# Optimization experiments

Hardware: AMD Instinct MI355X
Metric: run time of the kernel (lower is better)

The kernel has to match this reference:

```python
import jax, jax.numpy as jnp
import numpy as np

K = 20          # neighbors
T = 3           # time steps
GW = 10.0       # surrogate-gradient width
EPS = 1e-5      # batchnorm eps


def _knn_idx(f, k):
    # f: (B, N, C). torch code maximizes -||xi-xj||^2 via topk.
    x2 = jnp.sum(f * f, axis=-1)                          # (B, N)
    inner = jnp.einsum('bnc,bmc->bnm', f, f)              # (B, N, N)
    neg_d = 2.0 * inner - x2[:, :, None] - x2[:, None, :]
    return jax.lax.top_k(neg_d, k)[1]                     # (B, N, k)


def _graph_feature(f, k):
    # f: (B, N, C) -> (B, N, k, 2C) = cat(neighbor - center, neighbor)
    idx = _knn_idx(f, k)
    nb = jax.vmap(lambda ft, ix: ft[ix])(f, idx)          # (B, N, k, C)
    return jnp.concatenate([nb - f[:, :, None, :], nb], axis=-1)


def _bn(x, g, b, axes):
    # training-mode batchnorm (batch statistics), channel-last
    m = jnp.mean(x, axis=axes, keepdims=True)
    v = jnp.var(x, axis=axes, keepdims=True)
    return (x - m) * jax.lax.rsqrt(v + EPS) * g + b


def _lrelu(x):
    return jnp.where(x >= 0, x, 0.2 * x)


def _spike(x):
    # surrogate value + straight-through hard spike (training-mode detach trick)
    xc = jnp.clip(x, -10.0, 10.0)
    soft = 0.5 * jnp.exp(-0.5 * xc * xc) / np.sqrt(2.0 * np.pi) + 0.5 * jax.nn.sigmoid(GW * xc)
    hard = (x > 0).astype(x.dtype)
    return soft + jax.lax.stop_gradient(hard - soft)


def _lif(x, mem, thr, ref, md, ta, rd, tb):
    md = jnp.clip(md, 0.1, 0.99)
    ta = jnp.clip(ta, 0.001, 0.1)
    rd = jnp.clip(rd, 0.1, 0.95)
    x = x * (ref <= 0).astype(x.dtype)
    mem = mem * md * (1.0 - ref) + x
    s = _spike(mem - thr)
    mem = mem * (1.0 - s)
    ref = ref * rd + s
    thr = tb + (thr + ta * s - tb) * 0.95
    return s, mem, thr, ref


def _forward(x, W0, g0, b0, W1, g1, b1, W2, g2, b2, W3, g3, b3, Wm, gm, bm,
             l0md, l0ta, l0rd, l0tb, l1md, l1ta, l1rd, l1tb,
             l2md, l2ta, l2rd, l2tb, l3md, l3ta, l3rd, l3tb,
             lfmd, lfta, lfrd, lftb, tw):
    f0 = jnp.transpose(x, (0, 2, 1))                      # (B, N, 3)
    convs = [(W0, g0, b0), (W1, g1, b1), (W2, g2, b2), (W3, g3, b3)]
    lifs = [(l0md, l0ta, l0rd, l0tb), (l1md, l1ta, l1rd, l1tb),
            (l2md, l2ta, l2rd, l2tb), (l3md, l3ta, l3rd, l3tb)]
    states = [None] * 4
    pooled = []
    for t in range(T):
        cur = f0
        feats = []
        for i in range(4):
            gf = _graph_feature(cur, K)                   # (B, N, k, 2C)
            h = jnp.einsum('bnkc,oc->bnko', gf, convs[i][0])  # 1x1 conv
            h = _lrelu(_bn(h, convs[i][1], convs[i][2], (0, 1, 2)))
            h = jnp.max(h, axis=2)                        # max over k -> (B, N, O)
            md, ta, rd, tb = lifs[i]
            if states[i] is None:
                mem = jnp.zeros_like(h)
                thr = jnp.broadcast_to(tb, h.shape).astype(h.dtype)
                ref = jnp.zeros_like(h)
            else:
                # state manager detaches persisted states between calls
                mem, thr, ref = (jax.lax.stop_gradient(s) for s in states[i])
            s, mem, thr, ref = _lif(h, mem, thr, ref, md, ta, rd, tb)
            states[i] = (mem, thr, ref)
            feats.append(s)
            cur = s
        cat = jnp.concatenate(feats, axis=-1)             # (B, N, 960)
        agg = _lrelu(_bn(jnp.einsum('bnc,oc->bno', cat, Wm), gm, bm, (0, 1)))
        pooled.append(jnp.max(agg, axis=1))               # global max pool -> (B, 512)
    tf = jnp.stack(pooled, axis=0)                        # (T, B, 512)
    out = jnp.einsum('t,tbf->bf', jax.nn.softmax(tw), tf)
    mem = jnp.zeros_like(out)
    thr = jnp.broadcast_to(lftb, out.shape).astype(out.dtype)
    ref = jnp.zeros_like(out)
    s, _, _, _ = _lif(out, mem, thr, ref, lfmd, lfta, lfrd, lftb)
    return s


def setup_inputs() -> dict:
    key = jax.random.key(0)
    ks = iter(jax.random.split(key, 64))
    B, N = 2, 1024
    d = {}
    d['x'] = jax.random.normal(next(ks), (B, 3, N), jnp.float32)
    dims = [(64, 6), (128, 128), (256, 256), (512, 512)]  # (out, in) for 1x1 convs
    for i, (o, c) in enumerate(dims):
        d[f'W{i}'] = jax.random.normal(next(ks), (o, c), jnp.float32) / np.sqrt(c)
        d[f'g{i}'] = 1.0 + 0.1 * jax.random.normal(next(ks), (o,), jnp.float32)
        d[f'b{i}'] = 0.1 * jax.random.normal(next(ks), (o,), jnp.float32)
    d['Wm'] = jax.random.normal(next(ks), (512, 960), jnp.float32) / np.sqrt(960.0)
    d['gm'] = 1.0 + 0.1 * jax.random.normal(next(ks), (512,), jnp.float32)
    d['bm'] = 0.1 * jax.random.normal(next(ks), (512,), jnp.float32)
    for name, c in [('l0', 64), ('l1', 128), ('l2', 256), ('l3', 512), ('lf', 512)]:
        d[name + 'md'] = jnp.full((c,), 0.9, jnp.float32) + 0.02 * jax.random.normal(next(ks), (c,), jnp.float32)
        d[name + 'ta'] = jnp.full((c,), 0.01, jnp.float32) + 0.002 * jax.random.normal(next(ks), (c,), jnp.float32)
        d[name + 'rd'] = jnp.full((c,), 0.5, jnp.float32) + 0.02 * jax.random.normal(next(ks), (c,), jnp.float32)
        d[name + 'tb'] = jnp.ones((c,), jnp.float32) + 0.05 * jax.random.normal(next(ks), (c,), jnp.float32)
    d['tw'] = 1.0 + 0.1 * jax.random.normal(next(ks), (T,), jnp.float32)
    return d


def reference(x, W0, g0, b0, W1, g1, b1, W2, g2, b2, W3, g3, b3, Wm, gm, bm,
              l0md, l0ta, l0rd, l0tb, l1md, l1ta, l1rd, l1tb,
              l2md, l2ta, l2rd, l2tb, l3md, l3ta, l3rd, l3tb,
              lfmd, lfta, lfrd, lftb, tw):
    return _forward(x, W0, g0, b0, W1, g1, b1, W2, g2, b2, W3, g3, b3, Wm, gm, bm,
                    l0md, l0ta, l0rd, l0tb, l1md, l1ta, l1rd, l1tb,
                    l2md, l2ta, l2rd, l2tb, l3md, l3ta, l3rd, l3tb,
                    lfmd, lfta, lfrd, lftb, tw)
```

## Files before the change

kernel.cpp:

```cpp
#include <hip/hip_runtime.h>
#include <math.h>

#define NPTS 1024
#define BB 2
#define KNN 20
#define ROWS 2048
#define CATC 960
#define TT 3
#define IDXS 32
typedef unsigned long long ull;
typedef __attribute__((ext_vector_type(8))) short bf16x8;
typedef __attribute__((ext_vector_type(4))) float f32x4;

__device__ __forceinline__ float lrelu_f(float x){ return x >= 0.f ? x : 0.2f*x; }
__device__ __forceinline__ unsigned short f2bf(float f){
  unsigned u = __float_as_uint(f);
  return (unsigned short)((u + 0x7FFFu + ((u >> 16) & 1u)) >> 16);
}
__device__ __forceinline__ float bf2f(unsigned short h){ return __uint_as_float(((unsigned)h) << 16); }

__device__ __forceinline__ void stg_u32(unsigned* p, unsigned v){ __hip_atomic_store(p, v, __ATOMIC_RELAXED, __HIP_MEMORY_SCOPE_AGENT); }
__device__ __forceinline__ void stg_f64(double* p, double v){ __hip_atomic_store(p, v, __ATOMIC_RELAXED, __HIP_MEMORY_SCOPE_AGENT); }
__device__ __forceinline__ unsigned ldg_u32(const unsigned* p){ return __hip_atomic_load(p, __ATOMIC_RELAXED, __HIP_MEMORY_SCOPE_AGENT); }
__device__ __forceinline__ double ldg_f64(const double* p){ return __hip_atomic_load(p, __ATOMIC_RELAXED, __HIP_MEMORY_SCOPE_AGENT); }

__device__ __forceinline__ void mfma_dev(const short* __restrict__ A, int lda,
    const short* __restrict__ B3, size_t sStride, int ldb,
    float* __restrict__ C, int ldc, int K, int bm, int bn, int tid)
{
  const int wave = tid >> 6, lane = tid & 63;
  const int wm = (wave >> 1) << 5, wn = (wave & 1) << 5;
  const int rr = lane & 15, kq = (lane >> 4) << 3;
  f32x4 acc[2][2] = {};
  const short* Ap = A + (size_t)(bm + wm + rr)*lda + kq;
  const short* Bp = B3 + (size_t)(bn + wn + rr)*ldb + kq;
  for (int k0 = 0; k0 < K; k0 += 32) {
    bf16x8 a0 = *(const bf16x8*)(Ap + k0);
    bf16x8 a1 = *(const bf16x8*)(Ap + (size_t)16*lda + k0);
#pragma unroll
    for (int s = 0; s < 3; ++s) {
      bf16x8 b0 = *(const bf16x8*)(Bp + (size_t)s*sStride + k0);
      bf16x8 b1 = *(const bf16x8*)(Bp + (size_t)s*sStride + (size_t)16*ldb + k0);
      acc[0][0] = __builtin_amdgcn_mfma_f32_16x16x32_bf16(a0, b0, acc[0][0], 0, 0, 0);
      acc[0][1] = __builtin_amdgcn_mfma_f32_16x16x32_bf16(a0, b1, acc[0][1], 0, 0, 0);
      acc[1][0] = __builtin_amdgcn_mfma_f32_16x16x32_bf16(a1, b0, acc[1][0], 0, 0, 0);
      acc[1][1] = __builtin_amdgcn_mfma_f32_16x16x32_bf16(a1, b1, acc[1][1], 0, 0, 0);
    }
  }
  const int drb = (lane >> 4) << 2;
#pragma unroll
  for (int i = 0; i < 2; ++i)
#pragma unroll
    for (int j = 0; j < 2; ++j)
#pragma unroll
      for (int t = 0; t < 4; ++t)
        C[(size_t)(bm + wm + i*16 + drb + t)*ldc + bn + wn + j*16 + rr] = acc[i][j][t];
}

__device__ __forceinline__ void agg_tile64(const short* __restrict__ scat, const short* __restrict__ WmH,
    double* __restrict__ Sa1, double* __restrict__ Sa2, unsigned* __restrict__ mxe,
    int tm, int tn, int tid)
{
  const int wave = tid >> 6, lane = tid & 63;
  const int wm = (wave >> 1) << 5;
  const int wn = (wave & 1) << 5;
  const int rr = lane & 15, kq = (lane >> 4) << 3;
  const int bm = tm*64, bn = tn*64;
  f32x4 acc[2][2] = {};
  const short* Ap = scat + (size_t)(bm + wm + rr)*CATC + kq;
  const short* Bp = WmH + (size_t)(bn + wn + rr)*960 + kq;
  for (int k0 = 0; k0 < 960; k0 += 32){
    bf16x8 a0 = *(const bf16x8*)(Ap + k0);
    bf16x8 a1 = *(const bf16x8*)(Ap + (size_t)16*CATC + k0);
#pragma unroll
    for (int s = 0; s < 3; ++s){
      bf16x8 b0 = *(const bf16x8*)(Bp + (size_t)s*491520 + k0);
      bf16x8 b1 = *(const bf16x8*)(Bp + (size_t)s*491520 + (size_t)16*960 + k0);
      acc[0][0] = __builtin_amdgcn_mfma_f32_16x16x32_bf16(a0, b0, acc[0][0], 0, 0, 0);
      acc[0][1] = __builtin_amdgcn_mfma_f32_16x16x32_bf16(a0, b1, acc[0][1], 0, 0, 0);
      acc[1][0] = __builtin_amdgcn_mfma_f32_16x16x32_bf16(a1, b0, acc[1][0], 0, 0, 0);
      acc[1][1] = __builtin_amdgcn_mfma_f32_16x16x32_bf16(a1, b1, acc[1][1], 0, 0, 0);
    }
  }
#pragma unroll
  for (int j = 0; j < 2; ++j){
    double ds = 0.0, dq = 0.0; float mx = -INFINITY;
#pragma unroll
    for (int i = 0; i < 2; ++i)
#pragma unroll
      for (int t = 0; t < 4; ++t){
        float v = acc[i][j][t];
        ds += (double)v; dq += (double)v*(double)v; mx = fmaxf(mx, v);
      }
#pragma unroll
    for (int off = 16; off < 64; off <<= 1){
      ds += __shfl_xor(ds, off);
      dq += __shfl_xor(dq, off);
      float o = __shfl_xor(mx, off); mx = fmaxf(mx, o);
    }
    if (lane < 16){
      int col = bn + wn + j*16 + lane;
      atomicAdd(&Sa1[col], ds);
      atomicAdd(&Sa2[col], dq);
      unsigned u = __float_as_uint(mx);
      u = (u & 0x80000000u) ? ~u : (u | 0x80000000u);
      atomicMax(&mxe[(bm >> 10)*512 + col], u);
    }
  }
}

template<int W>
__device__ __forceinline__ void knn_wave(const ull* __restrict__ pk, int* __restrict__ idx,
                                         int row, int lane)
{
  const int n = row & (NPTS-1), b = row >> 10;
  const ull* pb = pk + (size_t)b*NPTS*W;
  ull cw[W]; int pn = 0;
#pragma unroll
  for (int w=0; w<W; ++w){ cw[w] = pb[(size_t)n*W + w]; pn += __popcll(cw[w]); }
  unsigned keys[16];
#pragma unroll 4
  for (int i=0;i<16;++i){
    int m = lane + (i<<6);
    int inner=0, pm=0;
#pragma unroll
    for (int w=0;w<W;++w){
      ull rm = pb[(size_t)m*W + w];
      inner += __popcll(rm & cw[w]);
      pm    += __popcll(rm);
    }
    int d = 2*inner - pn - pm;
    keys[i] = ((unsigned)(d+1024)<<11) | (unsigned)(NPTS-1-m);
  }
  unsigned lmax = keys[0];
#pragma unroll
  for (int i=1;i<16;++i) lmax = keys[i]>lmax ? keys[i] : lmax;
  unsigned mywin = 0;
  for (int s=0;s<KNN;++s){
    unsigned v = lmax;
#pragma unroll
    for (int off=1; off<64; off<<=1){ unsigned o = __shfl_xor(v, off, 64); if (o>v) v=o; }
    if (lane == s) mywin = (unsigned)(NPTS-1) - (v & 0x7FFu);
    if (lmax == v){
#pragma unroll
      for (int i=0;i<16;++i) if (keys[i]==v) keys[i]=0u;
      lmax = keys[0];
#pragma unroll
      for (int i=1;i<16;++i) lmax = keys[i]>lmax ? keys[i] : lmax;
    }
  }
  if (lane < KNN) idx[(size_t)row*IDXS + lane] = (int)mywin;
}

__device__ __forceinline__ void knn0_wave(const float* __restrict__ x, int* __restrict__ idx,
                                          int row, int lane)
{
  const int n = row & (NPTS-1), b = row >> 10;
  const float* xb = x + (size_t)b*3*NPTS;
  float fn0 = xb[n], fn1 = xb[NPTS+n], fn2 = xb[2*NPTS+n];
  float x2n = __fadd_rn(__fadd_rn(__fmul_rn(fn0,fn0), __fmul_rn(fn1,fn1)), __fmul_rn(fn2,fn2));
  ull keys[16];
#pragma unroll 4
  for (int i=0;i<16;++i){
    int m = lane + (i<<6);
    float a0 = xb[m], a1 = xb[NPTS+m], a2 = xb[2*NPTS+m];
    float x2m = __fadd_rn(__fadd_rn(__fmul_rn(a0,a0), __fmul_rn(a1,a1)), __fmul_rn(a2,a2));
    float inner = __fadd_rn(__fadd_rn(__fmul_rn(fn0,a0), __fmul_rn(fn1,a1)), __fmul_rn(fn2,a2));
    float v = __fsub_rn(__fsub_rn(__fmul_rn(2.f,inner), x2n), x2m);
    unsigned u = __float_as_uint(v);
    u = (u & 0x80000000u) ? ~u : (u | 0x80000000u);
    keys[i] = ((ull)u << 32) | (unsigned)(NPTS-1-m);
  }
  ull lmax = keys[0];
#pragma unroll
  for (int i=1;i<16;++i) lmax = keys[i]>lmax ? keys[i] : lmax;
  unsigned mywin = 0;
  for (int s=0;s<KNN;++s){
    ull v = lmax;
#pragma unroll
    for (int off=1; off<64; off<<=1){ ull o = __shfl_xor(v, off, 64); if (o>v) v=o; }
    if (lane == s) mywin = (unsigned)(NPTS-1) - (unsigned)(v & 0xFFFFFFFFull);
    if (lmax == v){
#pragma unroll
      for (int i=0;i<16;++i) if (keys[i]==v) keys[i]=0ull;
      lmax = keys[0];
#pragma unroll
      for (int i=1;i<16;++i) lmax = keys[i]>lmax ? keys[i] : lmax;
    }
  }
  if (lane < KNN) idx[(size_t)row*IDXS + lane] = (int)mywin;
}

__device__ __forceinline__ void conv0_dev(const float* __restrict__ x, const float* __restrict__ W0,
    float* __restrict__ AB0, int tile, int tid, float* sm)
{
  float (*As)[64] = (float(*)[64])sm;
  float (*Bs)[64] = (float(*)[64])(sm + 3*64);
  int bm = (tile >> 1) * 64, bn = (tile & 1) * 64;
  int b = bm >> 10, n0 = bm & (NPTS-1);
  if (tid < 192){ int k = tid >> 6, r = tid & 63; As[k][r] = x[(size_t)b*3072 + k*NPTS + n0 + r]; }
  if (tid >= 64){
    int k = (tid - 64) >> 6, c = (tid - 64) & 63; int row = bn + c;
    Bs[k][c] = (row < 64) ? __fadd_rn(W0[(size_t)row*6+k], W0[(size_t)row*6+3+k])
                          : W0[(size_t)(row-64)*6+k];
  }
  __syncthreads();
  const int tx = tid & 15, ty = tid >> 4;
  float acc[4][4] = {};
#pragma unroll
  for (int kk = 0; kk < 3; ++kk){
    float ar[4], br[4];
#pragma unroll
    for (int i=0;i<4;++i) ar[i] = As[kk][ty*4+i];
#pragma unroll
    for (int j=0;j<4;++j) br[j] = Bs[kk][tx*4+j];
#pragma unroll
    for (int i=0;i<4;++i)
#pragma unroll
      for (int j=0;j<4;++j) acc[i][j] = fmaf(ar[i], br[j], acc[i][j]);
  }
#pragma unroll
  for (int i=0;i<4;++i)
#pragma unroll
    for (int j=0;j<4;++j)
      AB0[(size_t)(bm+ty*4+i)*128 + bn+tx*4+j] = acc[i][j];
  __syncthreads();
}

__device__ __forceinline__ void wsplit_store(float w, short* dst, size_t NK, size_t e){
  unsigned short h1 = f2bf(w); float f1 = bf2f(h1);
  float r1 = w - f1;
  unsigned short h2 = f2bf(r1); float f2v = bf2f(h2);
  unsigned short h3 = f2bf(r1 - f2v);
  dst[e] = (short)h1; dst[NK + e] = (short)h2; dst[2*NK + e] = (short)h3;
}
__device__ __forceinline__ void wcatsplit(const float* __restrict__ W, short* __restrict__ dst,
                                          int O, int C, size_t e){
  int rr = (int)(e / C), cc = (int)(e - (size_t)rr*C);
  float w = (rr < O) ? __fadd_rn(W[(size_t)rr*2*C + cc], W[(size_t)rr*2*C + C + cc])
                     : W[(size_t)(rr-O)*2*C + cc];
  wsplit_store(w, dst, (size_t)2*O*C, e);
}

__device__ __forceinline__ float lif_step(float h, int o, size_t i, int init,
    double s1v, double s2v,
    const float* gv, const float* bv,
    const float* pmd, const float* pta, const float* prd, const float* ptb,
    float* sM, float* sT, float* sR)
{
  double cnt = (double)ROWS * (double)KNN;
  double mu = s1v / cnt;
  double vv = s2v / cnt - mu*mu;
  float mean = (float)mu;
  float inv  = 1.f / sqrtf((float)vv + 1e-5f);
  h = ((h - mean) * inv) * gv[o] + bv[o];
  h = lrelu_f(h);
  float md = fminf(fmaxf(pmd[o], 0.1f), 0.99f);
  float ta = fminf(fmaxf(pta[o], 0.001f), 0.1f);
  float rd = fminf(fmaxf(prd[o], 0.1f), 0.95f);
  float tb = ptb[o];
  float M, T, R;
  if (init) { M = 0.f; T = tb; R = 0.f; }
  else      { M = sM[i]; T = sT[i]; R = sR[i]; }
  float xv = (R <= 0.f) ? h : 0.f;
  M = M * md * (1.f - R) + xv;
  float sp = (M - T > 0.f) ? 1.f : 0.f;
  M = M * (1.f - sp);
  R = R * rd + sp;
  T = tb + (T + ta*sp - tb) * 0.95f;
  sM[i] = M; sT[i] = T; sR[i] = R;
  return sp;
}
__device__ __forceinline__ void emit_spike(float sp, short* scat, size_t row, int off, int o,
                                           ull* pk, size_t i, int tid)
{
  scat[row*CATC + off + o] = (sp != 0.f) ? (short)0x3F80 : (short)0;
  ull ball = __ballot(sp != 0.f);
  if ((tid & 63) == 0) pk[i >> 6] = ball;
}

__global__ __launch_bounds__(256) void k_setup(
    const float* W1, const float* W2, const float* W3, const float* Wm,
    short* wcH1, short* wcH2, short* wcH3, short* WmH,
    double* S12all, double* aggD, unsigned* aggM, unsigned* cnt)
{
  int vb = blockIdx.x, tid = threadIdx.x;
  if (vb < 10){ for (int j=tid; j<1024; j+=256) stg_f64(S12all + (size_t)vb*1024 + j, 0.0); }
  else if (vb < 13){ int t = vb-10;
    for (int j=tid; j<1024; j+=256){ stg_f64(aggD + (size_t)t*1024 + j, 0.0); stg_u32(aggM + (size_t)t*1024 + j, 0u); } }
  else if (vb < 14){ if (tid < 16) stg_u32(cnt + tid, 0u); }
  else if (vb < 78)   wcatsplit(W1, wcH1, 128,  64, (size_t)(vb-14)*256 + tid);
  else if (vb < 334)  wcatsplit(W2, wcH2, 256, 128, (size_t)(vb-78)*256 + tid);
  else if (vb < 1358) wcatsplit(W3, wcH3, 512, 256, (size_t)(vb-334)*256 + tid);
  else                wsplit_store(Wm[(size_t)(vb-1358)*256 + tid], WmH, (size_t)512*960, (size_t)(vb-1358)*256 + tid);
}

__global__ __launch_bounds__(256) void k_nt0(const float* __restrict__ x, const float* __restrict__ W0,
                                             int* __restrict__ idx0, float* __restrict__ AB0)
{
  __shared__ __align__(16) float sm[6*64];
  int bid = blockIdx.x, tid = threadIdx.x;
  if (bid < 512) knn0_wave(x, idx0, bid*4 + (tid>>6), tid & 63);
  else           conv0_dev(x, W0, AB0, bid - 512, tid, sm);
}

__global__ __launch_bounds__(256) void k_gather2(const float* __restrict__ AB, const int* __restrict__ idx,
    float* __restrict__ hmaxS, double* __restrict__ S12, int O, int OC, int RPB)
{
  __shared__ double red[2][4][64];
  const int bid = blockIdx.x, tid = threadIdx.x;
  const int wave = tid >> 6, lane = tid & 63;
  const int oc = bid % OC, rc = bid / OC;
  const int o = oc*64 + lane;
  const int twoO = 2*O;
  const int rstart = rc * RPB;
  double ts1 = 0.0, ts2 = 0.0;
  for (int r = rstart + wave; r < rstart + RPB; r += 4){
    int b = r >> 10;
    const float* ABb = AB + (size_t)(b*NPTS)*twoO + o;
    float bc = AB[(size_t)r*twoO + O + o];
    const int* ip = idx + (size_t)r*IDXS;
    float mx = -INFINITY; double s1 = 0.0, s2 = 0.0;
#pragma unroll
    for (int k = 0; k < KNN; ++k){
      int m = ip[k];
      float a = ABb[(size_t)m*twoO];
      mx = fmaxf(mx, a); s1 += (double)a; s2 += (double)a*(double)a;
    }
    hmaxS[(size_t)r*O + o] = mx - bc;
    ts1 += s1 - (double)KNN*(double)bc;
    ts2 += s2 - 2.0*(double)bc*s1 + (double)KNN*(double)bc*(double)bc;
  }
  red[0][wave][lane] = ts1;
  red[1][wave][lane] = ts2;
  __syncthreads();
  if (wave == 0){
    double a = red[0][0][lane] + red[0][1][lane] + red[0][2][lane] + red[0][3][lane];
    double q = red[1][0][lane] + red[1][1][lane] + red[1][2][lane] + red[1][3][lane];
    atomicAdd(&S12[o], a);
    atomicAdd(&S12[512 + o], q);
  }
}

__global__ __launch_bounds__(256) void k_lif0(const float* __restrict__ hmax0, const double* __restrict__ S12_0,
    const float* gv, const float* bv, const float* pmd, const float* pta, const float* prd, const float* ptb,
    float* sM, float* sT, float* sR, short* __restrict__ scat, ull* __restrict__ pk0)
{
  int i = blockIdx.x*256 + threadIdx.x, o = i & 63;
  size_t row = (size_t)(i >> 6);
  float sp = lif_step(hmax0[i], o, (size_t)i, 1, S12_0[o], S12_0[512+o],
                      gv, bv, pmd, pta, prd, ptb, sM, sT, sR);
  emit_spike(sp, scat, row, 0, o, pk0, (size_t)i, threadIdx.x);
}

template<int W>
__global__ __launch_bounds__(256) void k_knnconv(const ull* __restrict__ pk, int* __restrict__ idx,
    const short* __restrict__ Ain, const short* __restrict__ wcH,
    float* __restrict__ AB, int twoO, int K, int ntn,
    const short* __restrict__ scatPrev, const short* __restrict__ WmH,
    double* __restrict__ aggDt, unsigned* __restrict__ aggMt, int nMain)
{
  int bid = blockIdx.x, tid = threadIdx.x;
  if (bid < 512) knn_wave<W>(pk, idx, bid*4 + (tid>>6), tid & 63);
  else if (bid < nMain){
    int id = bid - 512, tm = id/ntn, tn = id - tm*ntn;
    mfma_dev(Ain, CATC, wcH, (size_t)twoO*K, K, AB, twoO, K, tm*64, tn*64, tid);
  } else {
    int tile = bid - nMain;
    agg_tile64(scatPrev, WmH, aggDt, aggDt + 512, aggMt, tile >> 3, tile & 7, tid);
  }
}

__global__ __launch_bounds__(256) void k_bnlif(const float* __restrict__ hmaxS, int oShift,
    const double* __restrict__ S12,
    const float* gv, const float* bv, const float* pmd, const float* pta, const float* prd, const float* ptb,
    float* sM, float* sT, float* sR, short* __restrict__ scat, int offOut,
    ull* __restrict__ pkOut, int init, int nMain,
    const float* __restrict__ hmax0, const double* __restrict__ S12_0,
    const float* g0, const float* b0, const float* pmd0, const float* pta0, const float* prd0, const float* ptb0,
    float* sM0, float* sT0, float* sR0, short* __restrict__ scatN, ull* __restrict__ pk0)
{
  int bid = blockIdx.x, tid = threadIdx.x;
  if (bid < nMain){
    int i = bid*256 + tid;
    int O = 1 << oShift;
    int o = i & (O-1);
    size_t row = (size_t)(i >> oShift);
    float sp = lif_step(hmaxS[i], o, (size_t)i, init, S12[o], S12[512+o],
                        gv, bv, pmd, pta, prd, ptb, sM, sT, sR);
    emit_spike(sp, scat, row, offOut, o, pkOut, (size_t)i, tid);
  } else {
    int i = (bid - nMain)*256 + tid, o = i & 63;
    size_t row = (size_t)(i >> 6);
    float sp = lif_step(hmax0[i], o, (size_t)i, 0, S12_0[o], S12_0[512+o],
                        g0, b0, pmd0, pta0, prd0, ptb0, sM0, sT0, sR0);
    emit_spike(sp, scatN, row, 0, o, pk0, (size_t)i, tid);
  }
}

__global__ __launch_bounds__(256) void k_aggfin(const short* __restrict__ scat2, const short* __restrict__ WmH,
    double* __restrict__ aggD, unsigned* __restrict__ aggM, unsigned* __restrict__ cnt,
    const float* gm, const float* bmv, const float* tw, const float* lftb, float* __restrict__ out)
{
  int bid = blockIdx.x, tid = threadIdx.x;
  if (bid < 256){
    agg_tile64(scat2, WmH, aggD + 2048, aggD + 2048 + 512, aggM + 2048, bid >> 3, bid & 7, tid);
    asm volatile("s_waitcnt vmcnt(0)" ::: "memory");
    __syncthreads();
    if (tid == 0) __hip_atomic_fetch_add(cnt, 1u, __ATOMIC_RELAXED, __HIP_MEMORY_SCOPE_AGENT);
  } else {
    if (tid == 0) while (ldg_u32(cnt) < 256u) __builtin_amdgcn_s_sleep(4);
    __syncthreads();
    int i = (bid - 256)*256 + tid;
    int b = i >> 9, o = i & 511;
    float pool[3];
#pragma unroll
    for (int t = 0; t < 3; ++t){
      double s1v = ldg_f64(&aggD[(size_t)t*1024 + o]);
      double s2v = ldg_f64(&aggD[(size_t)t*1024 + 512 + o]);
      double mean = s1v / (double)ROWS;
      float var = (float)(s2v / (double)ROWS - mean*mean);
      float m = (float)mean;
      float inv = 1.f / sqrtf(var + 1e-5f);
      unsigned e = ldg_u32(&aggM[(size_t)t*1024 + b*512 + o]);
      unsigned u = (e & 0x80000000u) ? (e & 0x7FFFFFFFu) : ~e;
      float mx = __uint_as_float(u);
      pool[t] = lrelu_f(((mx - m)*inv)*gm[o] + bmv[o]);
    }
    float t0 = tw[0], t1 = tw[1], t2 = tw[2];
    float mxw = fmaxf(t0, fmaxf(t1, t2));
    float e0 = expf(t0-mxw), e1 = expf(t1-mxw), e2 = expf(t2-mxw);
    float den = e0 + e1 + e2;
    float v = (e0/den)*pool[0] + (e1/den)*pool[1] + (e2/den)*pool[2];
    out[i] = (v - lftb[o] > 0.f) ? 1.f : 0.f;
  }
}

extern "C" void kernel_launch(void* const* d_in, const int* in_sizes, int n_in,
                              void* d_out, int out_size, void* d_ws, size_t ws_size,
                              hipStream_t stream)
{
  (void)in_sizes; (void)n_in; (void)out_size; (void)ws_size;
  const float* x = (const float*)d_in[0];
  const float* Wl[4] = {(const float*)d_in[1],(const float*)d_in[4],(const float*)d_in[7],(const float*)d_in[10]};
  const float* gl[4] = {(const float*)d_in[2],(const float*)d_in[5],(const float*)d_in[8],(const float*)d_in[11]};
  const float* bl[4] = {(const float*)d_in[3],(const float*)d_in[6],(const float*)d_in[9],(const float*)d_in[12]};
  const float* Wm = (const float*)d_in[13];
  const float* gm = (const float*)d_in[14];
  const float* bm = (const float*)d_in[15];
  const float* lp[5][4];
  for (int l = 0; l < 5; ++l)
    for (int q = 0; q < 4; ++q)
      lp[l][q] = (const float*)d_in[16 + l*4 + q];
  const float* tw = (const float*)d_in[36];

  char* pw = (char*)d_ws;
  auto alloc = [&](size_t bytes)->char* {
    char* r = pw; pw += (bytes + 255) & ~(size_t)255; return r;
  };
  int*    idx0  = (int*)   alloc((size_t)ROWS*IDXS*sizeof(int));
  int*    idxS  = (int*)   alloc((size_t)ROWS*IDXS*sizeof(int));
  float*  AB0   = (float*) alloc((size_t)ROWS*128*sizeof(float));
  float*  AB    = (float*) alloc((size_t)ROWS*1024*sizeof(float));
  float*  hmax0 = (float*) alloc((size_t)ROWS*64*sizeof(float));
  float*  hmaxS = (float*) alloc((size_t)ROWS*512*sizeof(float));
  double* S12   = (double*)alloc((size_t)10*1024*sizeof(double));
  short*  scatH[3];
  for (int t = 0; t < 3; ++t) scatH[t] = (short*)alloc((size_t)ROWS*CATC*sizeof(short));
  int Wn[4] = {1, 2, 4, 8};
  ull* pk[4];
  for (int l = 0; l < 4; ++l) pk[l] = (ull*)alloc((size_t)ROWS*Wn[l]*sizeof(ull));
  double*   aggD = (double*)  alloc((size_t)3*1024*sizeof(double));
  unsigned* aggM = (unsigned*)alloc((size_t)3*1024*sizeof(unsigned));
  short* wcH[4];
  wcH[1] = (short*)alloc((size_t)3*2*128*64*sizeof(short));
  wcH[2] = (short*)alloc((size_t)3*2*256*128*sizeof(short));
  wcH[3] = (short*)alloc((size_t)3*2*512*256*sizeof(short));
  short* WmH = (short*)alloc((size_t)3*512*960*sizeof(short));
  int Oo[4] = {64, 128, 256, 512};
  float *stM[4], *stT[4], *stR[4];
  for (int l = 0; l < 4; ++l){
    stM[l] = (float*)alloc((size_t)ROWS*Oo[l]*sizeof(float));
    stT[l] = (float*)alloc((size_t)ROWS*Oo[l]*sizeof(float));
    stR[l] = (float*)alloc((size_t)ROWS*Oo[l]*sizeof(float));
  }
  unsigned* cnt = (unsigned*)alloc(256);

  k_setup<<<3278, 256, 0, stream>>>(Wl[1], Wl[2], Wl[3], Wm,
                                    wcH[1], wcH[2], wcH[3], WmH, S12, aggD, aggM, cnt);
  k_nt0<<<576, 256, 0, stream>>>(x, Wl[0], idx0, AB0);
  k_gather2<<<512, 256, 0, stream>>>(AB0, idx0, hmax0, S12, 64, 1, 4);
  k_lif0<<<512, 256, 0, stream>>>(hmax0, S12, gl[0], bl[0],
      lp[0][0], lp[0][1], lp[0][2], lp[0][3],
      stM[0], stT[0], stR[0], scatH[0], pk[0]);

  int Cin[4]  = {3, 64, 128, 256};
  int offIn[4]= {0, 0, 64, 192};
  int offOut[4]={0, 64, 192, 448};

  for (int t = 0; t < TT; ++t){
    int init = (t == 0) ? 1 : 0;
    for (int li = 1; li < 4; ++li){
      int C = Cin[li], O = Oo[li], twoO = 2*O, ntn = twoO/64, nConv = 32*ntn;
      const short* fin = scatH[t] + offIn[li];
      double* S12i = S12 + (size_t)(1 + t*3 + (li-1))*1024;
      int nMain2 = 512 + nConv;
      int hasAgg = (li == 1 && t > 0) ? 1 : 0;
      int gridK = nMain2 + (hasAgg ? 256 : 0);
      const short* scPrev = hasAgg ? scatH[t-1] : (const short*)nullptr;
      double* aggDt = aggD + (size_t)(hasAgg ? (t-1) : 0)*1024;
      unsigned* aggMt = aggM + (size_t)(hasAgg ? (t-1) : 0)*1024;
      switch (Wn[li-1]){
        case 1: k_knnconv<1><<<gridK, 256, 0, stream>>>(pk[0], idxS, fin, wcH[li], AB, twoO, C, ntn,
                    scPrev, WmH, aggDt, aggMt, nMain2); break;
        case 2: k_knnconv<2><<<gridK, 256, 0, stream>>>(pk[1], idxS, fin, wcH[li], AB, twoO, C, ntn,
                    scPrev, WmH, aggDt, aggMt, nMain2); break;
        default: k_knnconv<4><<<gridK, 256, 0, stream>>>(pk[2], idxS, fin, wcH[li], AB, twoO, C, ntn,
                    scPrev, WmH, aggDt, aggMt, nMain2); break;
      }
      int OC = O/64;
      k_gather2<<<512, 256, 0, stream>>>(AB, idxS, hmaxS, S12i, O, OC, 4*OC);
      int oSh = (O==128)?7:(O==256)?8:9;
      int nMainB = (ROWS*O)/256;
      int tailLif0 = (li == 3 && t < 2) ? 512 : 0;
      k_bnlif<<<nMainB + tailLif0, 256, 0, stream>>>(hmaxS, oSh, S12i,
          gl[li], bl[li], lp[li][0], lp[li][1], lp[li][2], lp[li][3],
          stM[li], stT[li], stR[li], scatH[t], offOut[li], pk[li], init, nMainB,
          hmax0, S12, gl[0], bl[0], lp[0][0], lp[0][1], lp[0][2], lp[0][3],
          stM[0], stT[0], stR[0], (t < 2) ? scatH[t+1] : (short*)nullptr, pk[0]);
    }
  }
  k_aggfin<<<260, 256, 0, stream>>>(scatH[2], WmH, aggD, aggM, cnt + 9,
                                    gm, bm, tw, lp[4][3], (float*)d_out);
}
```

Measured before the change: 435.0 us.

## Fuse neighbor gather-max with batchnorm-LIF using a grid-wide counter barrier

The gather/max/statistics kernel is merged with the batchnorm+LIF spike kernel. Each block keeps its hmax tile in LDS, atomically accumulates the channel sums, then spins on a global counter until all 512 blocks have contributed, and applies BN and LIF locally. This removes one launch per layer and the hmaxS round trip through global memory. It relies on all 512 blocks being co-resident, since otherwise the spin barrier deadlocks, and it adds spin-wait latency. The extra tail blocks for the layer-0 LIF are placed after the barrier blocks and do not join the barrier.

```diff
diff --git a/kernel.cpp b/kernel.cpp
--- a/kernel.cpp
+++ b/kernel.cpp
@@ -271,13 +271,6 @@
   sM[i] = M; sT[i] = T; sR[i] = R;
   return sp;
 }
-__device__ __forceinline__ void emit_spike(float sp, short* scat, size_t row, int off, int o,
-                                           ull* pk, size_t i, int tid)
-{
-  scat[row*CATC + off + o] = (sp != 0.f) ? (short)0x3F80 : (short)0;
-  ull ball = __ballot(sp != 0.f);
-  if ((tid & 63) == 0) pk[i >> 6] = ball;
-}
 
 __global__ __launch_bounds__(256) void k_setup(
     const float* W1, const float* W2, const float* W3, const float* Wm,
@@ -288,7 +281,7 @@
   if (vb < 10){ for (int j=tid; j<1024; j+=256) stg_f64(S12all + (size_t)vb*1024 + j, 0.0); }
   else if (vb < 13){ int t = vb-10;
     for (int j=tid; j<1024; j+=256){ stg_f64(aggD + (size_t)t*1024 + j, 0.0); stg_u32(aggM + (size_t)t*1024 + j, 0u); } }
-  else if (vb < 14){ if (tid < 16) stg_u32(cnt + tid, 0u); }
+  else if (vb < 14){ if (tid < 32) stg_u32(cnt + tid, 0u); }
   else if (vb < 78)   wcatsplit(W1, wcH1, 128,  64, (size_t)(vb-14)*256 + tid);
   else if (vb < 334)  wcatsplit(W2, wcH2, 256, 128, (size_t)(vb-78)*256 + tid);
   else if (vb < 1358) wcatsplit(W3, wcH3, 512, 256, (size_t)(vb-334)*256 + tid);
@@ -304,11 +297,109 @@
   else           conv0_dev(x, W0, AB0, bid - 512, tid, sm);
 }
 
-__global__ __launch_bounds__(256) void k_gather2(const float* __restrict__ AB, const int* __restrict__ idx,
-    float* __restrict__ hmaxS, double* __restrict__ S12, int O, int OC, int RPB)
-{
-  __shared__ double red[2][4][64];
+struct GLds {
+  float hls[32*64];
+  double red[2][4][64];
+  double s1[64], s2[64];
+};
+
+__global__ __launch_bounds__(256) void k_gatherlif0(const float* __restrict__ AB0, const int* __restrict__ idx0,
+    float* __restrict__ hmax0, double* __restrict__ S12, unsigned* __restrict__ cnt,
+    const float* gv, const float* bv, const float* pmd, const float* pta, const float* prd, const float* ptb,
+    float* sM, float* sT, float* sR, short* __restrict__ scat, ull* __restrict__ pk0)
+{
+  __shared__ GLds L;
   const int bid = blockIdx.x, tid = threadIdx.x;
+  const int wave = tid >> 6, lane = tid & 63;
+  const int rstart = bid*4;
+  double ts1 = 0.0, ts2 = 0.0;
+  {
+    int r = rstart + wave;
+    int b = r >> 10;
+    const float* ABb = AB0 + (size_t)(b*NPTS)*128 + lane;
+    float bc = AB0[(size_t)r*128 + 64 + lane];
+    const int* ip = idx0 + (size_t)r*IDXS;
+    float mx = -INFINITY; double s1=0.0, s2=0.0;
+#pragma unroll
+    for (int k=0;k<KNN;++k){
+      int m = ip[k];
+      float a = ABb[(size_t)m*128];
+      mx = fmaxf(mx,a); s1 += (double)a; s2 += (double)a*(double)a;
+    }
+    float hv = mx - bc;
+    L.hls[wave*64 + lane] = hv;
+    hmax0[(size_t)r*64 + lane] = hv;
+    ts1 = s1 - (double)KNN*(double)bc;
+    ts2 = s2 - 2.0*(double)bc*s1 + (double)KNN*(double)bc*(double)bc;
+  }
+  L.red[0][wave][lane] = ts1;
+  L.red[1][wave][lane] = ts2;
+  __syncthreads();
+  if (wave == 0){
+    double a = L.red[0][0][lane]+L.red[0][1][lane]+L.red[0][2][lane]+L.red[0][3][lane];
+    double q = L.red[1][0][lane]+L.red[1][1][lane]+L.red[1][2][lane]+L.red[1][3][lane];
+    atomicAdd(&S12[lane], a);
+    atomicAdd(&S12[512 + lane], q);
+  }
+  __syncthreads();
+  if (tid == 0){
+    asm volatile("s_waitcnt vmcnt(0)" ::: "memory");
+    __hip_atomic_fetch_add(cnt, 1u, __ATOMIC_RELAXED, __HIP_MEMORY_SCOPE_AGENT);
+    while (ldg_u32(cnt) < 512u) __builtin_amdgcn_s_sleep(4);
+  }
+  __syncthreads();
+  if (tid < 64){ L.s1[tid] = ldg_f64(&S12[tid]); L.s2[tid] = ldg_f64(&S12[512+tid]); }
+  __syncthreads();
+  {
+    int r = rstart + wave;
+    size_t i = (size_t)r*64 + lane;
+    float sp = lif_step(L.hls[wave*64+lane], lane, i, 1, L.s1[lane], L.s2[lane],
+                        gv, bv, pmd, pta, prd, ptb, sM, sT, sR);
+    scat[(size_t)r*CATC + lane] = (sp != 0.f) ? (short)0x3F80 : (short)0;
+    ull ball = __ballot(sp != 0.f);
+    if (lane == 0) pk0[r] = ball;
+  }
+}
+
+template<int W>
+__global__ __launch_bounds__(256) void k_knnconv(const ull* __restrict__ pk, int* __restrict__ idx,
+    const short* __restrict__ Ain, const short* __restrict__ wcH,
+    float* __restrict__ AB, int twoO, int K, int ntn,
+    const short* __restrict__ scatPrev, const short* __restrict__ WmH,
+    double* __restrict__ aggDt, unsigned* __restrict__ aggMt, int nMain)
+{
+  int bid = blockIdx.x, tid = threadIdx.x;
+  if (bid < 512) knn_wave<W>(pk, idx, bid*4 + (tid>>6), tid & 63);
+  else if (bid < nMain){
+    int id = bid - 512, tm = id/ntn, tn = id - tm*ntn;
+    mfma_dev(Ain, CATC, wcH, (size_t)twoO*K, K, AB, twoO, K, tm*64, tn*64, tid);
+  } else {
+    int tile = bid - nMain;
+    agg_tile64(scatPrev, WmH, aggDt, aggDt + 512, aggMt, tile >> 3, tile & 7, tid);
+  }
+}
+
+__global__ __launch_bounds__(256) void k_gatherlif2(const float* __restrict__ AB, const int* __restrict__ idx,
+    double* __restrict__ S12, unsigned* __restrict__ cnt,
+    const float* gv, const float* bv, const float* pmd, const float* pta, const float* prd, const float* ptb,
+    float* sM, float* sT, float* sR, short* __restrict__ scat, int offOut,
+    ull* __restrict__ pkOut, int init, int O, int OC, int RPB,
+    const float* __restrict__ hmax0, const double* __restrict__ S12_0,
+    const float* g0, const float* b0, const float* pmd0, const float* pta0, const float* prd0, const float* ptb0,
+    float* sM0, float* sT0, float* sR0, short* __restrict__ scatN, ull* __restrict__ pk0)
+{
+  __shared__ GLds L;
+  const int bid = blockIdx.x, tid = threadIdx.x;
+  if (bid >= 512){
+    int i = (bid - 512)*256 + tid, o = i & 63;
+    size_t row = (size_t)(i >> 6);
+    float sp = lif_step(hmax0[i], o, (size_t)i, 0, S12_0[o], S12_0[512+o],
+                        g0, b0, pmd0, pta0, prd0, ptb0, sM0, sT0, sR0);
+    scatN[row*CATC + o] = (sp != 0.f) ? (short)0x3F80 : (short)0;
+    ull ball = __ballot(sp != 0.f);
+    if ((tid & 63) == 0) pk0[i >> 6] = ball;
+    return;
+  }
   const int wave = tid >> 6, lane = tid & 63;
   const int oc = bid % OC, rc = bid / OC;
   const int o = oc*64 + lane;
@@ -327,74 +418,37 @@
       float a = ABb[(size_t)m*twoO];
       mx = fmaxf(mx, a); s1 += (double)a; s2 += (double)a*(double)a;
     }
-    hmaxS[(size_t)r*O + o] = mx - bc;
+    L.hls[(r - rstart)*64 + lane] = mx - bc;
     ts1 += s1 - (double)KNN*(double)bc;
     ts2 += s2 - 2.0*(double)bc*s1 + (double)KNN*(double)bc*(double)bc;
   }
-  red[0][wave][lane] = ts1;
-  red[1][wave][lane] = ts2;
+  L.red[0][wave][lane] = ts1;
+  L.red[1][wave][lane] = ts2;
   __syncthreads();
   if (wave == 0){
-    double a = red[0][0][lane] + red[0][1][lane] + red[0][2][lane] + red[0][3][lane];
-    double q = red[1][0][lane] + red[1][1][lane] + red[1][2][lane] + red[1][3][lane];
+    double a = L.red[0][0][lane]+L.red[0][1][lane]+L.red[0][2][lane]+L.red[0][3][lane];
+    double q = L.red[1][0][lane]+L.red[1][1][lane]+L.red[1][2][lane]+L.red[1][3][lane];
     atomicAdd(&S12[o], a);
     atomicAdd(&S12[512 + o], q);
   }
-}
-
-__global__ __launch_bounds__(256) void k_lif0(const float* __restrict__ hmax0, const double* __restrict__ S12_0,
-    const float* gv, const float* bv, const float* pmd, const float* pta, const float* prd, const float* ptb,
-    float* sM, float* sT, float* sR, short* __restrict__ scat, ull* __restrict__ pk0)
-{
-  int i = blockIdx.x*256 + threadIdx.x, o = i & 63;
-  size_t row = (size_t)(i >> 6);
-  float sp = lif_step(hmax0[i], o, (size_t)i, 1, S12_0[o], S12_0[512+o],
-                      gv, bv, pmd, pta, prd, ptb, sM, sT, sR);
-  emit_spike(sp, scat, row, 0, o, pk0, (size_t)i, threadIdx.x);
-}
-
-template<int W>
-__global__ __launch_bounds__(256) void k_knnconv(const ull* __restrict__ pk, int* __restrict__ idx,
-    const short* __restrict__ Ain, const short* __restrict__ wcH,
-    float* __restrict__ AB, int twoO, int K, int ntn,
-    const short* __restrict__ scatPrev, const short* __restrict__ WmH,
-    double* __restrict__ aggDt, unsigned* __restrict__ aggMt, int nMain)
-{
-  int bid = blockIdx.x, tid = threadIdx.x;
-  if (bid < 512) knn_wave<W>(pk, idx, bid*4 + (tid>>6), tid & 63);
-  else if (bid < nMain){
-    int id = bid - 512, tm = id/ntn, tn = id - tm*ntn;
-    mfma_dev(Ain, CATC, wcH, (size_t)twoO*K, K, AB, twoO, K, tm*64, tn*64, tid);
-  } else {
-    int tile = bid - nMain;
-    agg_tile64(scatPrev, WmH, aggDt, aggDt + 512, aggMt, tile >> 3, tile & 7, tid);
-  }
-}
-
-__global__ __launch_bounds__(256) void k_bnlif(const float* __restrict__ hmaxS, int oShift,
-    const double* __restrict__ S12,
-    const float* gv, const float* bv, const float* pmd, const float* pta, const float* prd, const float* ptb,
-    float* sM, float* sT, float* sR, short* __restrict__ scat, int offOut,
-    ull* __restrict__ pkOut, int init, int nMain,
-    const float* __restrict__ hmax0, const double* __restrict__ S12_0,
-    const float* g0, const float* b0, const float* pmd0, const float* pta0, const float* prd0, const float* ptb0,
-    float* sM0, float* sT0, float* sR0, short* __restrict__ scatN, ull* __restrict__ pk0)
-{
-  int bid = blockIdx.x, tid = threadIdx.x;
-  if (bid < nMain){
-    int i = bid*256 + tid;
-    int O = 1 << oShift;
-    int o = i & (O-1);
-    size_t row = (size_t)(i >> oShift);
-    float sp = lif_step(hmaxS[i], o, (size_t)i, init, S12[o], S12[512+o],
+  __syncthreads();
+  if (tid == 0){
+    asm volatile("s_waitcnt vmcnt(0)" ::: "memory");
+    __hip_atomic_fetch_add(cnt, 1u, __ATOMIC_RELAXED, __HIP_MEMORY_SCOPE_AGENT);
+    while (ldg_u32(cnt) < 512u) __builtin_amdgcn_s_sleep(4);
+  }
+  __syncthreads();
+  if (tid < 64){ L.s1[tid] = ldg_f64(&S12[oc*64 + tid]); L.s2[tid] = ldg_f64(&S12[512 + oc*64 + tid]); }
+  __syncthreads();
+  for (int e = tid; e < RPB*64; e += 256){
+    int lr = e >> 6, lo = e & 63;
+    int r = rstart + lr;
+    size_t i = (size_t)r*O + oc*64 + lo;
+    float sp = lif_step(L.hls[e], lo, i, init, L.s1[lo], L.s2[lo],
                         gv, bv, pmd, pta, prd, ptb, sM, sT, sR);
-    emit_spike(sp, scat, row, offOut, o, pkOut, (size_t)i, tid);
-  } else {
-    int i = (bid - nMain)*256 + tid, o = i & 63;
-    size_t row = (size_t)(i >> 6);
-    float sp = lif_step(hmax0[i], o, (size_t)i, 0, S12_0[o], S12_0[512+o],
-                        g0, b0, pmd0, pta0, prd0, ptb0, sM0, sT0, sR0);
-    emit_spike(sp, scatN, row, 0, o, pk0, (size_t)i, tid);
+    scat[(size_t)r*CATC + offOut + oc*64 + lo] = (sp != 0.f) ? (short)0x3F80 : (short)0;
+    ull ball = __ballot(sp != 0.f);
+    if ((tid & 63) == 0) pkOut[(size_t)r*OC + oc] = ball;
   }
 }
 
@@ -463,7 +517,6 @@
   float*  AB0   = (float*) alloc((size_t)ROWS*128*sizeof(float));
   float*  AB    = (float*) alloc((size_t)ROWS*1024*sizeof(float));
   float*  hmax0 = (float*) alloc((size_t)ROWS*64*sizeof(float));
-  float*  hmaxS = (float*) alloc((size_t)ROWS*512*sizeof(float));
   double* S12   = (double*)alloc((size_t)10*1024*sizeof(double));
   short*  scatH[3];
   for (int t = 0; t < 3; ++t) scatH[t] = (short*)alloc((size_t)ROWS*CATC*sizeof(short));
@@ -489,9 +542,8 @@
   k_setup<<<3278, 256, 0, stream>>>(Wl[1], Wl[2], Wl[3], Wm,
                                     wcH[1], wcH[2], wcH[3], WmH, S12, aggD, aggM, cnt);
   k_nt0<<<576, 256, 0, stream>>>(x, Wl[0], idx0, AB0);
-  k_gather2<<<512, 256, 0, stream>>>(AB0, idx0, hmax0, S12, 64, 1, 4);
-  k_lif0<<<512, 256, 0, stream>>>(hmax0, S12, gl[0], bl[0],
-      lp[0][0], lp[0][1], lp[0][2], lp[0][3],
+  k_gatherlif0<<<512, 256, 0, stream>>>(AB0, idx0, hmax0, S12, cnt + 10,
+      gl[0], bl[0], lp[0][0], lp[0][1], lp[0][2], lp[0][3],
       stM[0], stT[0], stR[0], scatH[0], pk[0]);
 
   int Cin[4]  = {3, 64, 128, 256};
@@ -519,13 +571,10 @@
                     scPrev, WmH, aggDt, aggMt, nMain2); break;
       }
       int OC = O/64;
-      k_gather2<<<512, 256, 0, stream>>>(AB, idxS, hmaxS, S12i, O, OC, 4*OC);
-      int oSh = (O==128)?7:(O==256)?8:9;
-      int nMainB = (ROWS*O)/256;
       int tailLif0 = (li == 3 && t < 2) ? 512 : 0;
-      k_bnlif<<<nMainB + tailLif0, 256, 0, stream>>>(hmaxS, oSh, S12i,
+      k_gatherlif2<<<512 + tailLif0, 256, 0, stream>>>(AB, idxS, S12i, cnt + (t*3 + li - 1),
           gl[li], bl[li], lp[li][0], lp[li][1], lp[li][2], lp[li][3],
-          stM[li], stT[li], stR[li], scatH[t], offOut[li], pk[li], init, nMainB,
+          stM[li], stT[li], stR[li], scatH[t], offOut[li], pk[li], init, O, OC, 4*OC,
           hmax0, S12, gl[0], bl[0], lp[0][0], lp[0][1], lp[0][2], lp[0][3],
           stM[0], stT[0], stR[0], (t < 2) ? scatH[t+1] : (short*)nullptr, pk[0]);
     }
```

Result: slower. 602.4 us (+38.5%).
